# Optimization experiments

Hardware: AMD Instinct MI355X
Metric: run time of the kernel (lower is better)

## Reference

```python
import jax, jax.numpy as jnp
import numpy as np

D_MODEL, H, G, NPG = 2048, 256, 8, 512
B, N = 4, G * NPG


def _normalize(x, eps=1e-5):
    # F.normalize: x / max(||x||_2, eps) along last dim
    n = jnp.sqrt(jnp.sum(x * x, axis=-1, keepdims=True))
    return x / jnp.maximum(n, eps)


def _layernorm(x, g, b, eps=1e-5):
    mu = jnp.mean(x, axis=-1, keepdims=True)
    var = jnp.mean((x - mu) ** 2, axis=-1, keepdims=True)
    return (x - mu) * jax.lax.rsqrt(var + eps) * g + b


def setup_inputs() -> dict:
    key = jax.random.key(0)
    ks = jax.random.split(key, 12)
    s = 0.02
    return {
        "x": jax.random.normal(ks[0], (B, N, D_MODEL), jnp.float32),
        "M_prev": jax.random.normal(ks[1], (B, G, H, H), jnp.float32) * 0.1,
        "Wq": jax.random.normal(ks[2], (D_MODEL, H), jnp.float32) * s,
        "bq": jnp.zeros((H,), jnp.float32),
        "Wk": jax.random.normal(ks[3], (D_MODEL, H), jnp.float32) * s,
        "bk": jnp.zeros((H,), jnp.float32),
        "Wv": jax.random.normal(ks[4], (D_MODEL, H), jnp.float32) * s,
        "bv": jnp.zeros((H,), jnp.float32),
        "ln_g": jnp.ones((H,), jnp.float32),
        "ln_b": jnp.zeros((H,), jnp.float32),
        "Wo": jax.random.normal(ks[5], (H, D_MODEL), jnp.float32) * s,
        "bo": jnp.zeros((D_MODEL,), jnp.float32),
        "Wd": jax.random.normal(ks[6], (D_MODEL, 1), jnp.float32) * s,
        "bd": jnp.zeros((1,), jnp.float32),
        "timescale": jnp.linspace(-3.0, 8.0, G).reshape(1, G, 1).astype(jnp.float32),
    }


def reference(x, M_prev, Wq, bq, Wk, bk, Wv, bv, ln_g, ln_b, Wo, bo, Wd, bd, timescale):
    q = _normalize(x @ Wq + bq)                      # [B,N,H]
    k = _normalize(x @ Wk + bk)                      # [B,N,H]
    v = _layernorm(x @ Wv + bv, ln_g, ln_b)          # [B,N,H]

    BG = B * G
    M_f = M_prev.reshape(BG, H, H)
    k_f = k.reshape(BG, NPG, H)
    v_f = v.reshape(BG, NPG, H)
    q_f = q.reshape(BG, NPG, H)

    # v_pred = k @ M^T   [BG,NPG,H]
    v_pred = jnp.einsum('bnh,bmh->bnm', k_f, M_f)
    surprise = v_f - v_pred
    # delta_M = surprise^T @ k / NPG   [BG,H,H]
    delta_M = jnp.einsum('bnm,bnh->bmh', surprise, k_f) / NPG

    gamma = jax.nn.sigmoid(
        (x @ Wd + bd).reshape(B, G, NPG, 1).mean(axis=2) + timescale
    )[..., None]                                     # [B,G,1,1]

    M_next = jnp.clip(gamma * M_prev + delta_M.reshape(B, G, H, H), -10.0, 10.0)

    out_f = jnp.einsum('bnh,bmh->bnm', q_f, M_next.reshape(BG, H, H))  # [BG,NPG,H]
    out = out_f.reshape(B, N, H) @ Wo + bo
    return out, M_next
```

## Files before the change

kernel.cpp:

```cpp
#include <hip/hip_runtime.h>
#include <stdint.h>

typedef __bf16 bf16;
typedef bf16  bf16x4 __attribute__((ext_vector_type(4)));
typedef bf16  bf16x8 __attribute__((ext_vector_type(8)));
typedef float f32x4  __attribute__((ext_vector_type(4)));

__device__ __forceinline__ void gll16(const void* g, void* l) {
  __builtin_amdgcn_global_load_lds(
      (__attribute__((address_space(1))) void*)g,
      (__attribute__((address_space(3))) void*)l, 16, 0, 0);
}

__global__ __launch_bounds__(256) void k_prep(
    const float* __restrict__ Wq, const float* __restrict__ Wk, const float* __restrict__ Wv,
    const float* __restrict__ Wo, const float* __restrict__ Mp, const float* __restrict__ x,
    const float* __restrict__ Wd,
    bf16* __restrict__ Wt, bf16* __restrict__ WoT, bf16* __restrict__ Mb,
    bf16* __restrict__ xb, float* __restrict__ rowdot) {
  __shared__ float tle[32][33];
  const int id = blockIdx.x, t = threadIdx.x;
  if (id < 1536) {
    const float* src = id < 512 ? Wq : (id < 1024 ? Wk : Wv);
    bf16* dst = Wt + (size_t)(id / 512) * 256 * 2048;
    int lid = id & 511;
    int r0 = (lid >> 3) * 32, c0 = (lid & 7) * 32;
    int i = t >> 5, j = t & 31;
#pragma unroll
    for (int p = 0; p < 4; p++) tle[i + 8 * p][j] = src[(size_t)(r0 + i + 8 * p) * 256 + c0 + j];
    __syncthreads();
#pragma unroll
    for (int p = 0; p < 4; p++)
      dst[(size_t)(c0 + i + 8 * p) * 2048 + r0 + j] = (bf16)tle[j][i + 8 * p];
  } else if (id < 2048) {
    int lid = id - 1536;
    int r0 = (lid >> 6) * 32, c0 = (lid & 63) * 32;
    int i = t >> 5, j = t & 31;
#pragma unroll
    for (int p = 0; p < 4; p++) tle[i + 8 * p][j] = Wo[(size_t)(r0 + i + 8 * p) * 2048 + c0 + j];
    __syncthreads();
#pragma unroll
    for (int p = 0; p < 4; p++)
      WoT[(size_t)(c0 + i + 8 * p) * 256 + r0 + j] = (bf16)tle[j][i + 8 * p];
  } else if (id < 4096) {
    int i = (id - 2048) * 256 + t;
    f32x4 v = *(const f32x4*)(Mp + (size_t)i * 4);
    bf16x4 o; o[0] = (bf16)v[0]; o[1] = (bf16)v[1]; o[2] = (bf16)v[2]; o[3] = (bf16)v[3];
    *(bf16x4*)(Mb + (size_t)i * 4) = o;
  } else {
    const int lane = t & 63, w = t >> 6;
    const int row = (id - 4096) * 4 + w;
    const float* xp = x + (size_t)row * 2048;
    bf16* op = xb + (size_t)row * 2048;
    float dot = 0.f;
#pragma unroll
    for (int u = 0; u < 8; u++) {
      int off = u * 256 + lane * 4;
      f32x4 v  = *(const f32x4*)(xp + off);
      f32x4 wv = *(const f32x4*)(Wd + off);
      dot += v[0] * wv[0] + v[1] * wv[1] + v[2] * wv[2] + v[3] * wv[3];
      bf16x4 o; o[0] = (bf16)v[0]; o[1] = (bf16)v[1]; o[2] = (bf16)v[2]; o[3] = (bf16)v[3];
      *(bf16x4*)(op + off) = o;
    }
#pragma unroll
    for (int s = 32; s; s >>= 1) dot += __shfl_xor(dot, s);
    if (lane == 0) rowdot[row] = dot;
  }
}

__global__ __launch_bounds__(512) void k_qkv(const bf16* __restrict__ xb,
    const bf16* __restrict__ Wt,
    const float* __restrict__ bq, const float* __restrict__ bk, const float* __restrict__ bv,
    const float* __restrict__ lng, const float* __restrict__ lnb,
    bf16* __restrict__ qkvh) {
  __shared__ bf16 As[2][4096];
  __shared__ bf16 Bs[2][8192];
  __shared__ float red1[512], red2[512];
  const int t = threadIdx.x, lane = t & 63, w = t >> 6;
  const int sec = blockIdx.y;
  const int row0 = blockIdx.x * 128, n0 = sec * 256;
  const int wr = (w & 1) * 64, wc = (w >> 1) * 64;
  const int l15 = lane & 15, ql = lane >> 4;
  f32x4 acc[4][4] = {};

  auto STAGE = [&](int buf, int kt) {
    const int kb = kt * 32;
    { int r = t >> 2, gl = (t & 3) ^ ((r >> 1) & 3);
      gll16(xb + (size_t)(row0 + r) * 2048 + kb + gl * 8, &As[buf][(t & ~63) * 8]); }
#pragma unroll
    for (int i = 0; i < 2; i++) {
      int s = i * 512 + t;
      int r = s >> 2, gl = (s & 3) ^ ((r >> 1) & 3);
      gll16(Wt + (size_t)(n0 + r) * 2048 + kb + gl * 8, &Bs[buf][(i * 512 + (t & ~63)) * 8]);
    }
  };
  auto COMPUTE = [&](int buf) {
    bf16x8 af[4], bfv[4];
#pragma unroll
    for (int m = 0; m < 4; m++) {
      int ra = wr + m * 16 + l15;
      af[m] = *(const bf16x8*)&As[buf][ra * 32 + ((ql ^ ((ra >> 1) & 3)) << 3)];
    }
#pragma unroll
    for (int n = 0; n < 4; n++) {
      int rb = wc + n * 16 + l15;
      bfv[n] = *(const bf16x8*)&Bs[buf][rb * 32 + ((ql ^ ((rb >> 1) & 3)) << 3)];
    }
#pragma unroll
    for (int m = 0; m < 4; m++)
#pragma unroll
      for (int n = 0; n < 4; n++)
        acc[m][n] = __builtin_amdgcn_mfma_f32_16x16x32_bf16(af[m], bfv[n], acc[m][n], 0, 0, 0);
  };

  STAGE(0, 0);
  int cur = 0;
  for (int tt = 0; tt < 64; ++tt) {
    if (tt < 63) {
      STAGE(cur ^ 1, tt + 1);
      asm volatile("s_waitcnt vmcnt(3)" ::: "memory");
    } else {
      asm volatile("s_waitcnt vmcnt(0)" ::: "memory");
    }
    __builtin_amdgcn_s_barrier();
    COMPUTE(cur);
    __builtin_amdgcn_s_barrier();
    cur ^= 1;
  }

  __syncthreads();
  const float* bias = sec == 0 ? bq : (sec == 1 ? bk : bv);
#pragma unroll
  for (int m = 0; m < 4; m++)
#pragma unroll
    for (int j = 0; j < 4; j++) {
      float p1 = 0.f, p2 = 0.f;
#pragma unroll
      for (int n = 0; n < 4; n++) {
        float v = acc[m][n][j] + bias[wc + n * 16 + l15];
        p1 += v; p2 += v * v;
      }
#pragma unroll
      for (int mask = 8; mask; mask >>= 1) {
        p1 += __shfl_xor(p1, mask);
        p2 += __shfl_xor(p2, mask);
      }
      if (l15 == 0) {
        int rl = wr + m * 16 + ql * 4 + j;
        red1[rl * 4 + (w >> 1)] = p1;
        red2[rl * 4 + (w >> 1)] = p2;
      }
    }
  __syncthreads();
#pragma unroll
  for (int m = 0; m < 4; m++)
#pragma unroll
    for (int j = 0; j < 4; j++) {
      int rl = wr + m * 16 + ql * 4 + j;
      float s1 = red1[rl * 4] + red1[rl * 4 + 1] + red1[rl * 4 + 2] + red1[rl * 4 + 3];
      float s2 = red2[rl * 4] + red2[rl * 4 + 1] + red2[rl * 4 + 2] + red2[rl * 4 + 3];
      float sc = 1.f / fmaxf(sqrtf(s2), 1e-5f);
      float mu = s1 * (1.f / 256.f);
      float rs = rsqrtf(s2 * (1.f / 256.f) - mu * mu + 1e-5f);
#pragma unroll
      for (int n = 0; n < 4; n++) {
        int c = wc + n * 16 + l15;
        float v = acc[m][n][j] + bias[c];
        float o = sec < 2 ? v * sc : (v - mu) * rs * lng[c] + lnb[c];
        qkvh[(size_t)(row0 + rl) * 768 + n0 + c] = (bf16)o;
      }
    }
}

__global__ __launch_bounds__(256) void k_gamma(const float* __restrict__ rowdot,
    const float* __restrict__ bd, const float* __restrict__ ts, float* __restrict__ gamma) {
  __shared__ float red[256];
  const int t = threadIdx.x, bg = blockIdx.x;
  red[t] = rowdot[bg * 512 + t] + rowdot[bg * 512 + 256 + t];
  __syncthreads();
  if (t < 64) {
    float s = red[t] + red[t + 64] + red[t + 128] + red[t + 192];
#pragma unroll
    for (int sh = 32; sh; sh >>= 1) s += __shfl_down(s, sh);
    if (t == 0) gamma[bg] = 1.f / (1.f + expf(-(s * (1.f / 512.f) + bd[0] + ts[bg & 7])));
  }
}

__global__ __launch_bounds__(512) void k_qM(const bf16* __restrict__ qkvh,
    const bf16* __restrict__ M, bf16* __restrict__ out, int sec, int dosub) {
  __shared__ bf16 Al[2][4096];
  __shared__ bf16 Bl[2][4096];
  const int t = threadIdx.x, lane = t & 63, w = t >> 6;
  const int bg = blockIdx.x, nb = blockIdx.y, mb = blockIdx.z;
  const int row0 = bg * 512 + nb * 128, m0 = mb * 128;
  const int wrow = (w & 1) * 64, wcol = (w >> 1) * 32;
  const int l15 = lane & 15, ql = lane >> 4;
  f32x4 acc[4][2] = {};

  auto STAGE = [&](int buf, int kt) {
    const int kb = kt * 32;
    int r = t >> 2, gl = (t & 3) ^ ((r >> 1) & 3);
    gll16(qkvh + (size_t)(row0 + r) * 768 + sec + kb + gl * 8, &Al[buf][(t & ~63) * 8]);
    gll16(M + (size_t)bg * 65536 + (size_t)(m0 + r) * 256 + kb + gl * 8, &Bl[buf][(t & ~63) * 8]);
  };
  auto COMPUTE = [&](int buf) {
    bf16x8 af[4], bfv[2];
#pragma unroll
    for (int m = 0; m < 4; m++) {
      int ra = wrow + m * 16 + l15;
      af[m] = *(const bf16x8*)&Al[buf][ra * 32 + ((ql ^ ((ra >> 1) & 3)) << 3)];
    }
#pragma unroll
    for (int n = 0; n < 2; n++) {
      int rb = wcol + n * 16 + l15;
      bfv[n] = *(const bf16x8*)&Bl[buf][rb * 32 + ((ql ^ ((rb >> 1) & 3)) << 3)];
    }
#pragma unroll
    for (int m = 0; m < 4; m++)
#pragma unroll
      for (int n = 0; n < 2; n++)
        acc[m][n] = __builtin_amdgcn_mfma_f32_16x16x32_bf16(af[m], bfv[n], acc[m][n], 0, 0, 0);
  };

  STAGE(0, 0);
  int cur = 0;
  for (int tt = 0; tt < 8; ++tt) {
    if (tt < 7) {
      STAGE(cur ^ 1, tt + 1);
      asm volatile("s_waitcnt vmcnt(2)" ::: "memory");
    } else {
      asm volatile("s_waitcnt vmcnt(0)" ::: "memory");
    }
    __builtin_amdgcn_s_barrier();
    COMPUTE(cur);
    __builtin_amdgcn_s_barrier();
    cur ^= 1;
  }
#pragma unroll
  for (int m = 0; m < 4; m++)
#pragma unroll
    for (int n = 0; n < 2; n++)
#pragma unroll
      for (int j = 0; j < 4; j++) {
        int gr = row0 + wrow + m * 16 + ql * 4 + j;
        int c = m0 + wcol + n * 16 + l15;
        float val = acc[m][n][j];
        if (dosub) val = (float)qkvh[(size_t)gr * 768 + 512 + c] - val;
        out[(size_t)gr * 256 + c] = (bf16)val;
      }
}

__global__ __launch_bounds__(512) void k_deltaM(const bf16* __restrict__ s,
    const bf16* __restrict__ qkvh, const float* __restrict__ Mp,
    const float* __restrict__ gamma, float* __restrict__ Mnext, bf16* __restrict__ Mnb) {
  __shared__ bf16 Sl[2][8192];
  __shared__ bf16 Kl[2][4096];
  const int t = threadIdx.x, lane = t & 63, w = t >> 6;
  const int bg = blockIdx.x;
  const int m0 = blockIdx.y * 128, h0 = blockIdx.z * 64;
  const int wm = (w & 3) * 32, wh = (w >> 2) * 32;
  const int l15 = lane & 15, g8 = (lane >> 4) * 8;
  const int nl = t & 63, cj = t >> 6;
  f32x4 acc[2][2] = {};

  bf16x8 vs0, vs1, vk;
  auto LOADREGS = [&](int kb) {
    vs0 = *(const bf16x8*)(s + (size_t)(bg * 512 + kb + nl) * 256 + m0 + cj * 8);
    vs1 = *(const bf16x8*)(s + (size_t)(bg * 512 + kb + nl) * 256 + m0 + 64 + cj * 8);
    vk  = *(const bf16x8*)(qkvh + (size_t)(bg * 512 + kb + nl) * 768 + 256 + h0 + cj * 8);
  };
  auto DSWRITE = [&](int buf) {
#pragma unroll
    for (int e = 0; e < 8; e++) {
      int m = cj * 8 + e;
      Sl[buf][m * 64 + (nl ^ ((m & 7) * 8))] = vs0[e];
      int m2 = m + 64;
      Sl[buf][m2 * 64 + (nl ^ ((m2 & 7) * 8))] = vs1[e];
      Kl[buf][m * 64 + (nl ^ ((m & 7) * 8))] = vk[e];
    }
  };

  LOADREGS(0);
  DSWRITE(0);
  __syncthreads();
  int cur = 0;
  for (int it = 0; it < 8; ++it) {
    if (it < 7) LOADREGS((it + 1) * 64);
#pragma unroll
    for (int kk = 0; kk < 64; kk += 32) {
      bf16x8 af[2], bfv[2];
#pragma unroll
      for (int m = 0; m < 2; m++) {
        int ml = wm + m * 16 + l15;
        af[m] = *(const bf16x8*)&Sl[cur][ml * 64 + ((kk + g8) ^ ((ml & 7) * 8))];
      }
#pragma unroll
      for (int n = 0; n < 2; n++) {
        int hl = wh + n * 16 + l15;
        bfv[n] = *(const bf16x8*)&Kl[cur][hl * 64 + ((kk + g8) ^ ((hl & 7) * 8))];
      }
#pragma unroll
      for (int m = 0; m < 2; m++)
#pragma unroll
        for (int n = 0; n < 2; n++)
          acc[m][n] = __builtin_amdgcn_mfma_f32_16x16x32_bf16(af[m], bfv[n], acc[m][n], 0, 0, 0);
    }
    if (it < 7) DSWRITE(cur ^ 1);
    __syncthreads();
    cur ^= 1;
  }
  const float gm = gamma[bg];
#pragma unroll
  for (int m = 0; m < 2; m++)
#pragma unroll
    for (int n = 0; n < 2; n++)
#pragma unroll
      for (int j = 0; j < 4; j++) {
        int mg = m0 + wm + m * 16 + (lane >> 4) * 4 + j;
        int hg = h0 + wh + n * 16 + l15;
        size_t idx = (size_t)bg * 65536 + (size_t)mg * 256 + hg;
        float val = gm * Mp[idx] + acc[m][n][j] * (1.f / 512.f);
        val = fminf(10.f, fmaxf(-10.f, val));
        Mnext[idx] = val;
        Mnb[idx] = (bf16)val;
      }
}

__global__ __launch_bounds__(512) void k_out(const bf16* __restrict__ outf,
    const bf16* __restrict__ WoT, const float* __restrict__ bo, float* __restrict__ out) {
  __shared__ bf16 As[2][4096];
  __shared__ bf16 Bs[2][8192];
  const int t = threadIdx.x, lane = t & 63, w = t >> 6;
  const int row0 = blockIdx.x * 128, n0 = blockIdx.y * 256;
  const int wr = (w & 1) * 64, wc = (w >> 1) * 64;
  const int l15 = lane & 15, ql = lane >> 4;
  f32x4 acc[4][4] = {};

  auto STAGE = [&](int buf, int kt) {
    const int kb = kt * 32;
    { int r = t >> 2, gl = (t & 3) ^ ((r >> 1) & 3);
      gll16(outf + (size_t)(row0 + r) * 256 + kb + gl * 8, &As[buf][(t & ~63) * 8]); }
#pragma unroll
    for (int i = 0; i < 2; i++) {
      int s = i * 512 + t;
      int r = s >> 2, gl = (s & 3) ^ ((r >> 1) & 3);
      gll16(WoT + (size_t)(n0 + r) * 256 + kb + gl * 8, &Bs[buf][(i * 512 + (t & ~63)) * 8]);
    }
  };
  auto COMPUTE = [&](int buf) {
    bf16x8 af[4], bfv[4];
#pragma unroll
    for (int m = 0; m < 4; m++) {
      int ra = wr + m * 16 + l15;
      af[m] = *(const bf16x8*)&As[buf][ra * 32 + ((ql ^ ((ra >> 1) & 3)) << 3)];
    }
#pragma unroll
    for (int n = 0; n < 4; n++) {
      int rb = wc + n * 16 + l15;
      bfv[n] = *(const bf16x8*)&Bs[buf][rb * 32 + ((ql ^ ((rb >> 1) & 3)) << 3)];
    }
#pragma unroll
    for (int m = 0; m < 4; m++)
#pragma unroll
      for (int n = 0; n < 4; n++)
        acc[m][n] = __builtin_amdgcn_mfma_f32_16x16x32_bf16(af[m], bfv[n], acc[m][n], 0, 0, 0);
  };

  STAGE(0, 0);
  int cur = 0;
  for (int tt = 0; tt < 8; ++tt) {
    if (tt < 7) {
      STAGE(cur ^ 1, tt + 1);
      asm volatile("s_waitcnt vmcnt(3)" ::: "memory");
    } else {
      asm volatile("s_waitcnt vmcnt(0)" ::: "memory");
    }
    __builtin_amdgcn_s_barrier();
    COMPUTE(cur);
    __builtin_amdgcn_s_barrier();
    cur ^= 1;
  }
#pragma unroll
  for (int m = 0; m < 4; m++)
#pragma unroll
    for (int n = 0; n < 4; n++)
#pragma unroll
      for (int j = 0; j < 4; j++) {
        int r = row0 + wr + m * 16 + ql * 4 + j;
        int c = n0 + wc + n * 16 + l15;
        out[(size_t)r * 2048 + c] = acc[m][n][j] + bo[c];
      }
}

extern "C" void kernel_launch(void* const* d_in, const int* in_sizes, int n_in,
                              void* d_out, int out_size, void* d_ws, size_t ws_size,
                              hipStream_t stream) {
  const float* x   = (const float*)d_in[0];
  const float* Mp  = (const float*)d_in[1];
  const float* Wq  = (const float*)d_in[2];
  const float* bq  = (const float*)d_in[3];
  const float* Wk  = (const float*)d_in[4];
  const float* bk  = (const float*)d_in[5];
  const float* Wv  = (const float*)d_in[6];
  const float* bv  = (const float*)d_in[7];
  const float* lng = (const float*)d_in[8];
  const float* lnb = (const float*)d_in[9];
  const float* Wo  = (const float*)d_in[10];
  const float* bo  = (const float*)d_in[11];
  const float* Wd  = (const float*)d_in[12];
  const float* bd  = (const float*)d_in[13];
  const float* ts  = (const float*)d_in[14];

  char* ws = (char*)d_ws;
  bf16*  Wt     = (bf16*)(ws);
  bf16*  WoT    = (bf16*)(ws + 3145728);
  bf16*  Mb     = (bf16*)(ws + 4194304);
  bf16*  qkvh   = (bf16*)(ws + 8388608);
  bf16*  sbuf   = (bf16*)(ws + 33554432);
  bf16*  Mnb    = (bf16*)(ws + 41943040);
  bf16*  outf   = (bf16*)(ws + 46137344);
  float* rowdot = (float*)(ws + 54525952);
  float* gamma  = (float*)(ws + 54591488);

  float* out   = (float*)d_out;
  float* Mnext = (float*)d_out + 33554432;
  bf16*  xb    = (bf16*)d_out;

  dim3 b256(256), b512(512);
  k_prep<<<dim3(8192),       b256, 0, stream>>>(Wq, Wk, Wv, Wo, Mp, x, Wd, Wt, WoT, Mb, xb, rowdot);
  k_qkv<<<dim3(128, 3),      b512, 0, stream>>>(xb, Wt, bq, bk, bv, lng, lnb, qkvh);
  k_gamma<<<dim3(32),        b256, 0, stream>>>(rowdot, bd, ts, gamma);
  k_qM<<<dim3(32, 4, 2),     b512, 0, stream>>>(qkvh, Mb, sbuf, 256, 1);
  k_deltaM<<<dim3(32, 2, 4), b512, 0, stream>>>(sbuf, qkvh, Mp, gamma, Mnext, Mnb);
  k_qM<<<dim3(32, 4, 2),     b512, 0, stream>>>(qkvh, Mnb, outf, 0, 0);
  k_out<<<dim3(128, 8),      b512, 0, stream>>>(outf, WoT, bo, out);
}
```

Baseline: 199.8 us.

## Fuse x bf16 conversion and gate rowdot into QKV GEMM loads

Drops the separate prep pass that converted x to bf16 and computed the x·Wd row dot. The QKV GEMM now streams fp32 x straight into LDS with a new swizzle, converts it to bf16 in registers before the MFMA, and the first section also accumulates the gate dot product from the same tiles. This avoids writing and re-reading a 32MB bf16 copy of x, but doubles the A-tile LDS footprint and global load traffic per GEMM block, since x is read in fp32 by all three sections. It also adds conversion work to the inner loop.

```diff
diff --git a/kernel.cpp b/kernel.cpp
--- a/kernel.cpp
+++ b/kernel.cpp
@@ -14,10 +14,8 @@
 
 __global__ __launch_bounds__(256) void k_prep(
     const float* __restrict__ Wq, const float* __restrict__ Wk, const float* __restrict__ Wv,
-    const float* __restrict__ Wo, const float* __restrict__ Mp, const float* __restrict__ x,
-    const float* __restrict__ Wd,
-    bf16* __restrict__ Wt, bf16* __restrict__ WoT, bf16* __restrict__ Mb,
-    bf16* __restrict__ xb, float* __restrict__ rowdot) {
+    const float* __restrict__ Wo, const float* __restrict__ Mp,
+    bf16* __restrict__ Wt, bf16* __restrict__ WoT, bf16* __restrict__ Mb) {
   __shared__ float tle[32][33];
   const int id = blockIdx.x, t = threadIdx.x;
   if (id < 1536) {
@@ -42,56 +40,50 @@
 #pragma unroll
     for (int p = 0; p < 4; p++)
       WoT[(size_t)(c0 + i + 8 * p) * 256 + r0 + j] = (bf16)tle[j][i + 8 * p];
-  } else if (id < 4096) {
+  } else {
     int i = (id - 2048) * 256 + t;
     f32x4 v = *(const f32x4*)(Mp + (size_t)i * 4);
     bf16x4 o; o[0] = (bf16)v[0]; o[1] = (bf16)v[1]; o[2] = (bf16)v[2]; o[3] = (bf16)v[3];
     *(bf16x4*)(Mb + (size_t)i * 4) = o;
-  } else {
-    const int lane = t & 63, w = t >> 6;
-    const int row = (id - 4096) * 4 + w;
-    const float* xp = x + (size_t)row * 2048;
-    bf16* op = xb + (size_t)row * 2048;
-    float dot = 0.f;
-#pragma unroll
-    for (int u = 0; u < 8; u++) {
-      int off = u * 256 + lane * 4;
-      f32x4 v  = *(const f32x4*)(xp + off);
-      f32x4 wv = *(const f32x4*)(Wd + off);
-      dot += v[0] * wv[0] + v[1] * wv[1] + v[2] * wv[2] + v[3] * wv[3];
-      bf16x4 o; o[0] = (bf16)v[0]; o[1] = (bf16)v[1]; o[2] = (bf16)v[2]; o[3] = (bf16)v[3];
-      *(bf16x4*)(op + off) = o;
-    }
-#pragma unroll
-    for (int s = 32; s; s >>= 1) dot += __shfl_xor(dot, s);
-    if (lane == 0) rowdot[row] = dot;
-  }
-}
-
-__global__ __launch_bounds__(512) void k_qkv(const bf16* __restrict__ xb,
-    const bf16* __restrict__ Wt,
+  }
+}
+
+__global__ __launch_bounds__(512) void k_qkv(const float* __restrict__ x,
+    const bf16* __restrict__ Wt, const float* __restrict__ Wd,
     const float* __restrict__ bq, const float* __restrict__ bk, const float* __restrict__ bv,
     const float* __restrict__ lng, const float* __restrict__ lnb,
-    bf16* __restrict__ qkvh) {
-  __shared__ bf16 As[2][4096];
-  __shared__ bf16 Bs[2][8192];
+    bf16* __restrict__ qkvh, float* __restrict__ rowdot) {
+  __shared__ float Asf[2][4096];
+  __shared__ bf16  Bs[2][8192];
+  __shared__ float WdL[2048];
   __shared__ float red1[512], red2[512];
   const int t = threadIdx.x, lane = t & 63, w = t >> 6;
   const int sec = blockIdx.y;
   const int row0 = blockIdx.x * 128, n0 = sec * 256;
   const int wr = (w & 1) * 64, wc = (w >> 1) * 64;
   const int l15 = lane & 15, ql = lane >> 4;
+  const int rt = t >> 2, qt = t & 3;
   f32x4 acc[4][4] = {};
+  float dot = 0.f;
+
+  if (sec == 0) *(f32x4*)&WdL[t * 4] = *(const f32x4*)(Wd + t * 4);
+  __syncthreads();
 
   auto STAGE = [&](int buf, int kt) {
     const int kb = kt * 32;
-    { int r = t >> 2, gl = (t & 3) ^ ((r >> 1) & 3);
-      gll16(xb + (size_t)(row0 + r) * 2048 + kb + gl * 8, &As[buf][(t & ~63) * 8]); }
+#pragma unroll
+    for (int i = 0; i < 2; i++) {
+      int s = i * 512 + t;
+      int r = s >> 3, gl = (s & 7) ^ (r & 7);
+      gll16(x + (size_t)(row0 + r) * 2048 + kb + gl * 4,
+            &Asf[buf][(i * 512 + (t & ~63)) * 4]);
+    }
 #pragma unroll
     for (int i = 0; i < 2; i++) {
       int s = i * 512 + t;
       int r = s >> 2, gl = (s & 3) ^ ((r >> 1) & 3);
-      gll16(Wt + (size_t)(n0 + r) * 2048 + kb + gl * 8, &Bs[buf][(i * 512 + (t & ~63)) * 8]);
+      gll16(Wt + (size_t)(n0 + r) * 2048 + kb + gl * 8,
+            &Bs[buf][(i * 512 + (t & ~63)) * 8]);
     }
   };
   auto COMPUTE = [&](int buf) {
@@ -99,7 +91,13 @@
 #pragma unroll
     for (int m = 0; m < 4; m++) {
       int ra = wr + m * 16 + l15;
-      af[m] = *(const bf16x8*)&As[buf][ra * 32 + ((ql ^ ((ra >> 1) & 3)) << 3)];
+      int g0 = (2 * ql) ^ (ra & 7), g1 = (2 * ql + 1) ^ (ra & 7);
+      f32x4 a0 = *(const f32x4*)&Asf[buf][ra * 32 + g0 * 4];
+      f32x4 a1 = *(const f32x4*)&Asf[buf][ra * 32 + g1 * 4];
+      bf16x8 o;
+#pragma unroll
+      for (int e = 0; e < 4; e++) { o[e] = (bf16)a0[e]; o[4 + e] = (bf16)a1[e]; }
+      af[m] = o;
     }
 #pragma unroll
     for (int n = 0; n < 4; n++) {
@@ -111,6 +109,16 @@
 #pragma unroll
       for (int n = 0; n < 4; n++)
         acc[m][n] = __builtin_amdgcn_mfma_f32_16x16x32_bf16(af[m], bfv[n], acc[m][n], 0, 0, 0);
+  };
+  auto ROWDOT = [&](int buf, int kt) {
+    const int kb = kt * 32;
+    int g0 = (2 * qt) ^ (rt & 7), g1 = (2 * qt + 1) ^ (rt & 7);
+    f32x4 d0 = *(const f32x4*)&Asf[buf][rt * 32 + g0 * 4];
+    f32x4 d1 = *(const f32x4*)&Asf[buf][rt * 32 + g1 * 4];
+    f32x4 w0 = *(const f32x4*)&WdL[kb + qt * 8];
+    f32x4 w1 = *(const f32x4*)&WdL[kb + qt * 8 + 4];
+    dot += d0[0] * w0[0] + d0[1] * w0[1] + d0[2] * w0[2] + d0[3] * w0[3]
+         + d1[0] * w1[0] + d1[1] * w1[1] + d1[2] * w1[2] + d1[3] * w1[3];
   };
 
   STAGE(0, 0);
@@ -118,14 +126,21 @@
   for (int tt = 0; tt < 64; ++tt) {
     if (tt < 63) {
       STAGE(cur ^ 1, tt + 1);
-      asm volatile("s_waitcnt vmcnt(3)" ::: "memory");
+      asm volatile("s_waitcnt vmcnt(4)" ::: "memory");
     } else {
       asm volatile("s_waitcnt vmcnt(0)" ::: "memory");
     }
     __builtin_amdgcn_s_barrier();
     COMPUTE(cur);
+    if (sec == 0) ROWDOT(cur, tt);
     __builtin_amdgcn_s_barrier();
     cur ^= 1;
+  }
+
+  if (sec == 0) {
+    dot += __shfl_xor(dot, 1);
+    dot += __shfl_xor(dot, 2);
+    if (qt == 0) rowdot[row0 + rt] = dot;
   }
 
   __syncthreads();
@@ -424,11 +439,10 @@
 
   float* out   = (float*)d_out;
   float* Mnext = (float*)d_out + 33554432;
-  bf16*  xb    = (bf16*)d_out;
 
   dim3 b256(256), b512(512);
-  k_prep<<<dim3(8192),       b256, 0, stream>>>(Wq, Wk, Wv, Wo, Mp, x, Wd, Wt, WoT, Mb, xb, rowdot);
-  k_qkv<<<dim3(128, 3),      b512, 0, stream>>>(xb, Wt, bq, bk, bv, lng, lnb, qkvh);
+  k_prep<<<dim3(4096),       b256, 0, stream>>>(Wq, Wk, Wv, Wo, Mp, Wt, WoT, Mb);
+  k_qkv<<<dim3(128, 3),      b512, 0, stream>>>(x, Wt, Wd, bq, bk, bv, lng, lnb, qkvh, rowdot);
   k_gamma<<<dim3(32),        b256, 0, stream>>>(rowdot, bd, ts, gamma);
   k_qM<<<dim3(32, 4, 2),     b512, 0, stream>>>(qkvh, Mb, sbuf, 256, 1);
   k_deltaM<<<dim3(32, 2, 4), b512, 0, stream>>>(sbuf, qkvh, Mp, gamma, Mnext, Mnb);
```

New measurement: 251.9 us. +26.1%, slower.
